# Optimization experiments

Hardware: AMD Instinct MI355X
Metric: run time of the kernel (lower is better)

## Reference

```python
import jax, jax.numpy as jnp
import numpy as np

E = 512      # embed_dim
H = 8        # num_heads
D = E // H   # head_dim = 64
R = 32       # rot_dims (partial rotary)
THETA = 10000.0


def _rope(x):
    # x: [B, H, S, D]; rotate first R dims (interleaved pairs, lucidrains-style)
    S = x.shape[-2]
    inv_freq = THETA ** (-jnp.arange(0, R, 2, dtype=jnp.float32) / R)  # [R/2]
    ang = jnp.arange(S, dtype=jnp.float32)[:, None] * inv_freq          # [S, R/2]
    c, s = jnp.cos(ang), jnp.sin(ang)
    xr, xp = x[..., :R], x[..., R:]
    x1, x2 = xr[..., 0::2], xr[..., 1::2]
    rot = jnp.stack([x1 * c - x2 * s, x1 * s + x2 * c], axis=-1).reshape(xr.shape)
    return jnp.concatenate([rot, xp], axis=-1)


def setup_inputs() -> dict:
    key = jax.random.key(0)
    k1, k2, k3, k4 = jax.random.split(key, 4)
    B, S = 4, 2048
    x = jax.random.normal(k1, (B, S, E), dtype=jnp.float32)
    input_mask = jax.random.randint(k2, (B, S), 0, 2).astype(bool)
    W_in = jax.random.normal(k3, (3 * E, E), dtype=jnp.float32) / np.sqrt(E).astype(np.float32)
    W_out = jax.random.normal(k4, (E, E), dtype=jnp.float32) / np.sqrt(E).astype(np.float32)
    return {"x": x, "input_mask": input_mask, "W_in": W_in, "W_out": W_out}


def reference(x, input_mask, W_in, W_out):
    B, S, _ = x.shape
    # fused QKV projection (Linear, no bias): x @ W_in.T -> [B,S,3E]
    qkv = (x @ W_in.T).reshape(B, S, 3, H, D).transpose(2, 0, 3, 1, 4)  # [3,B,H,S,D]
    q, k, v = qkv[0], qkv[1], qkv[2]
    q = _rope(q)
    k = _rope(k)
    # mask: causal AND (both tokens valid OR diagonal)
    causal = jnp.tril(jnp.ones((S, S), dtype=bool))
    inv = ~input_mask                                  # [B,S]
    cross = inv[:, None, :] | inv[:, :, None]          # [B,S,S]
    square = (~cross) | jnp.eye(S, dtype=bool)         # diagonal forced True
    full = causal[None, :, :] & square                 # [B,S,S]
    scores = jnp.einsum('bhsd,bhtd->bhst', q, k) / np.float32(np.sqrt(D))
    scores = jnp.where(full[:, None, :, :], scores, -jnp.inf)
    probs = jax.nn.softmax(scores, axis=-1)
    attn = jnp.einsum('bhst,bhtd->bhsd', probs, v)
    attn = attn.transpose(0, 2, 1, 3).reshape(B, S, E)
    return attn @ W_out.T
```

## Files before the change

kernel.cpp:

```cpp
#include <hip/hip_runtime.h>
#include <math.h>

#define B_ 4
#define S_ 2048
#define E_ 512
#define H_ 8
#define D_ 64

typedef short bf16x8 __attribute__((ext_vector_type(8)));
typedef float f32x4 __attribute__((ext_vector_type(4)));

__device__ inline short f2bf(float f) {
  union { float f; unsigned u; } v; v.f = f;
  unsigned r = v.u + 0x7FFF + ((v.u >> 16) & 1);
  return (short)(r >> 16);
}
__device__ inline short f2bf_fast(float f) {
  union { float f; unsigned u; } v; v.f = f;
  return (short)((v.u + 0x8000u) >> 16);
}
__device__ inline float bf2f(short s) {
  union { unsigned u; float f; } v; v.u = ((unsigned)(unsigned short)s) << 16;
  return v.f;
}

__global__ __launch_bounds__(256) void cvt_bf16(const float* __restrict__ src,
                                                short* __restrict__ dst, int n4) {
  int i = blockIdx.x * 256 + threadIdx.x;
  if (i < n4) {
    float4 f = ((const float4*)src)[i];
    short4 o;
    o.x = f2bf(f.x); o.y = f2bf(f.y); o.z = f2bf(f.z); o.w = f2bf(f.w);
    ((short4*)dst)[i] = o;
  }
}

__global__ __launch_bounds__(256) void gemm_qkv_mfma(
    const short* __restrict__ Xb,
    const short* __restrict__ Wb,
    short* __restrict__ qb, short* __restrict__ kb, short* __restrict__ vbT) {
  __shared__ __align__(16) short As[128][40];
  __shared__ __align__(16) short Bs[128][40];
  const int tid = threadIdx.x;
  const int w = tid >> 6, lane = tid & 63;
  const int l15 = lane & 15, quad = lane >> 4;
  const int wm = w & 1, wn = w >> 1;
  const int m0 = blockIdx.x * 128;
  const int n0 = blockIdx.y * 128;
  f32x4 acc[4][4];
  for (int mt = 0; mt < 4; ++mt)
    for (int nt = 0; nt < 4; ++nt) acc[mt][nt] = (f32x4){0.f, 0.f, 0.f, 0.f};

  for (int k0 = 0; k0 < E_; k0 += 32) {
    __syncthreads();
    for (int l = 0; l < 2; ++l) {
      int c = tid + 256 * l;
      int row = c >> 2, k8 = (c & 3) * 8;
      *(bf16x8*)&As[row][k8] = *(const bf16x8*)&Xb[(size_t)(m0 + row) * E_ + k0 + k8];
      *(bf16x8*)&Bs[row][k8] = *(const bf16x8*)&Wb[(size_t)(n0 + row) * E_ + k0 + k8];
    }
    __syncthreads();
    bf16x8 a[4], bfr[4];
    for (int mt = 0; mt < 4; ++mt)
      a[mt] = *(const bf16x8*)&As[wm * 64 + mt * 16 + l15][quad * 8];
    for (int nt = 0; nt < 4; ++nt)
      bfr[nt] = *(const bf16x8*)&Bs[wn * 64 + nt * 16 + l15][quad * 8];
    for (int mt = 0; mt < 4; ++mt)
      for (int nt = 0; nt < 4; ++nt)
        acc[mt][nt] = __builtin_amdgcn_mfma_f32_16x16x32_bf16(a[mt], bfr[nt], acc[mt][nt], 0, 0, 0);
  }
  const int t3 = n0 >> 9;
  for (int nt = 0; nt < 4; ++nt) {
    const int n = n0 + wn * 64 + nt * 16 + l15;
    const int h = (n >> 6) & 7;
    const int d = n & 63;
    const bool dorope = (t3 < 2) && (d < 32);
    const float sgn = (d & 1) ? 1.f : -1.f;
    const float fr = dorope ? powf(10000.f, -(float)(2 * (d >> 1)) * (1.f / 32.f)) : 0.f;
    for (int mt = 0; mt < 4; ++mt) {
      for (int i = 0; i < 4; ++i) {
        const int m = m0 + wm * 64 + mt * 16 + quad * 4 + i;
        const int b = m >> 11, s = m & (S_ - 1);
        float val = acc[mt][nt][i];
        float pv = __shfl_xor(val, 1, 64);
        float outv = val;
        if (dorope) {
          float ang = (float)s * fr;
          float sn, cs;
          sincosf(ang, &sn, &cs);
          outv = val * cs + pv * sgn * sn;
        }
        if (t3 == 2)
          vbT[((size_t)(b * 8 + h) * D_ + d) * S_ + s] = f2bf(outv);
        else {
          short* dst = (t3 == 0) ? qb : kb;
          dst[(((size_t)(b * 8 + h)) * S_ + s) * D_ + d] = f2bf(outv);
        }
      }
    }
  }
}

__global__ __launch_bounds__(256) void gemm_out_mfma(
    const short* __restrict__ Ab, const short* __restrict__ Wb,
    float* __restrict__ out) {
  __shared__ __align__(16) short As[128][40];
  __shared__ __align__(16) short Bs[128][40];
  const int tid = threadIdx.x;
  const int w = tid >> 6, lane = tid & 63;
  const int l15 = lane & 15, quad = lane >> 4;
  const int wm = w & 1, wn = w >> 1;
  const int m0 = blockIdx.x * 128;
  const int n0 = blockIdx.y * 128;
  f32x4 acc[4][4];
  for (int mt = 0; mt < 4; ++mt)
    for (int nt = 0; nt < 4; ++nt) acc[mt][nt] = (f32x4){0.f, 0.f, 0.f, 0.f};

  for (int k0 = 0; k0 < E_; k0 += 32) {
    __syncthreads();
    for (int l = 0; l < 2; ++l) {
      int c = tid + 256 * l;
      int row = c >> 2, k8 = (c & 3) * 8;
      *(bf16x8*)&As[row][k8] = *(const bf16x8*)&Ab[(size_t)(m0 + row) * E_ + k0 + k8];
      *(bf16x8*)&Bs[row][k8] = *(const bf16x8*)&Wb[(size_t)(n0 + row) * E_ + k0 + k8];
    }
    __syncthreads();
    bf16x8 a[4], bfr[4];
    for (int mt = 0; mt < 4; ++mt)
      a[mt] = *(const bf16x8*)&As[wm * 64 + mt * 16 + l15][quad * 8];
    for (int nt = 0; nt < 4; ++nt)
      bfr[nt] = *(const bf16x8*)&Bs[wn * 64 + nt * 16 + l15][quad * 8];
    for (int mt = 0; mt < 4; ++mt)
      for (int nt = 0; nt < 4; ++nt)
        acc[mt][nt] = __builtin_amdgcn_mfma_f32_16x16x32_bf16(a[mt], bfr[nt], acc[mt][nt], 0, 0, 0);
  }
  for (int mt = 0; mt < 4; ++mt)
    for (int nt = 0; nt < 4; ++nt) {
      const int n = n0 + wn * 64 + nt * 16 + l15;
      for (int i = 0; i < 4; ++i) {
        const int m = m0 + wm * 64 + mt * 16 + quad * 4 + i;
        out[(size_t)m * E_ + n] = acc[mt][nt][i];
      }
    }
}

__global__ __launch_bounds__(256) void flash_mfma(
    const short* __restrict__ qb, const short* __restrict__ kb,
    const short* __restrict__ vbT, const int* __restrict__ maskp,
    short* __restrict__ pb0, short* __restrict__ pb1,
    float* __restrict__ lb0, float* __restrict__ lb1,
    short* __restrict__ ob) {
  __shared__ __align__(16) short Ks[64][72];
  __shared__ __align__(16) short VT[64][72];
  __shared__ __align__(16) short Pl[4][16][72];
  __shared__ float kbias[64];
  const int tid = threadIdx.x;
  const int w = tid >> 6, lane = tid & 63;
  const int l15 = lane & 15, quad = lane >> 4;
  const int bid = blockIdx.x;
  const int u = bid & 7, v = bid >> 3;
  const int bh = (u << 2) | (v & 3);
  const int w2 = v >> 2;
  const int pair = w2 & 15;
  const int kh = w2 >> 4;
  const int b = bh >> 3, hd = bh & 7;
  const short* qbase = qb + (size_t)bh * S_ * D_;
  const short* kbase = kb + (size_t)bh * S_ * D_;
  const short* vtb   = vbT + (size_t)bh * D_ * S_;
  short* PB = kh ? pb1 : pb0;
  float* LB = kh ? lb1 : lb0;
  const float c2 = 0.1803368801f;
  bf16x8 ones;
  for (int j = 0; j < 8; ++j) ones[j] = (short)0x3F80;

  for (int seg = 0; seg < 2; ++seg) {
    const int qt = (seg == 0) ? pair : 31 - pair;
    const int r0 = qt * 64;
    const int mid = (qt + 2) >> 1;
    const int lo = kh ? mid : 0;
    const int hi = kh ? (qt + 1) : mid;
    bf16x8 aq[2];
    {
      const short* qrow = qbase + (size_t)(r0 + 16 * w + l15) * D_;
      aq[0] = *(const bf16x8*)&qrow[quad * 8];
      aq[1] = *(const bf16x8*)&qrow[32 + quad * 8];
    }
    f32x4 o[4], lsum;
    for (int no = 0; no < 4; ++no) o[no] = (f32x4){0.f, 0.f, 0.f, 0.f};
    lsum = (f32x4){0.f, 0.f, 0.f, 0.f};

    for (int kt = lo; kt < hi; ++kt) {
      const int t0 = kt * 64;
      __syncthreads();
      for (int l = 0; l < 2; ++l) {
        int idx = tid + 256 * l;
        int row = idx >> 3, ch = (idx & 7) * 8;
        *(bf16x8*)&Ks[row][ch] = *(const bf16x8*)(kbase + (size_t)(t0 + row) * D_ + ch);
        *(bf16x8*)&VT[row][ch] = *(const bf16x8*)(vtb + (size_t)row * S_ + t0 + ch);
      }
      if (tid < 64)
        kbias[tid] = maskp[b * S_ + t0 + tid] ? -23.08312f : -1.0e38f;
      __syncthreads();
      f32x4 sfr[4];
      for (int nb = 0; nb < 4; ++nb) sfr[nb] = (f32x4){0.f, 0.f, 0.f, 0.f};
      for (int nb = 0; nb < 4; ++nb)
        for (int ks = 0; ks < 2; ++ks) {
          bf16x8 bk = *(const bf16x8*)&Ks[l15 + 16 * nb][32 * ks + quad * 8];
          sfr[nb] = __builtin_amdgcn_mfma_f32_16x16x32_bf16(aq[ks], bk, sfr[nb], 0, 0, 0);
        }
      if (kt < qt) {
        for (int nb = 0; nb < 4; ++nb) {
          const float bb = kbias[l15 + 16 * nb];
          for (int i = 0; i < 4; ++i)
            Pl[w][quad * 4 + i][l15 + 16 * nb] = f2bf_fast(exp2f(sfr[nb][i] * c2 + bb));
        }
      } else {
        for (int nb = 0; nb < 4; ++nb) {
          const int tg = l15 + 16 * nb;
          const float bb = kbias[l15 + 16 * nb];
          for (int i = 0; i < 4; ++i) {
            const float bbi = (tg > 16 * w + quad * 4 + i) ? -1.0e38f : bb;
            Pl[w][quad * 4 + i][l15 + 16 * nb] = f2bf_fast(exp2f(sfr[nb][i] * c2 + bbi));
          }
        }
      }
      asm volatile("s_waitcnt lgkmcnt(0)" ::: "memory");
      bf16x8 ap0 = *(const bf16x8*)&Pl[w][l15][quad * 8];
      bf16x8 ap1 = *(const bf16x8*)&Pl[w][l15][32 + quad * 8];
      for (int no = 0; no < 4; ++no) {
        bf16x8 bv0 = *(const bf16x8*)&VT[16 * no + l15][quad * 8];
        bf16x8 bv1 = *(const bf16x8*)&VT[16 * no + l15][32 + quad * 8];
        o[no] = __builtin_amdgcn_mfma_f32_16x16x32_bf16(ap0, bv0, o[no], 0, 0, 0);
        o[no] = __builtin_amdgcn_mfma_f32_16x16x32_bf16(ap1, bv1, o[no], 0, 0, 0);
      }
      lsum = __builtin_amdgcn_mfma_f32_16x16x32_bf16(ap0, ones, lsum, 0, 0, 0);
      lsum = __builtin_amdgcn_mfma_f32_16x16x32_bf16(ap1, ones, lsum, 0, 0, 0);
    }
    for (int i = 0; i < 4; ++i) {
      const int s = r0 + 16 * w + quad * 4 + i;
      const int qm = maskp[b * S_ + s];
      const size_t row = (size_t)(b * S_ + s) * E_ + hd * D_;
      if (kh == 0 && !qm) {
        for (int no = 0; no < 4; ++no) {
          const int d = l15 + 16 * no;
          ob[row + d] = vtb[(size_t)d * S_ + s];
        }
      }
      for (int no = 0; no < 4; ++no)
        PB[row + l15 + 16 * no] = f2bf(o[no][i]);
      if (l15 == 0)
        LB[bh * S_ + s] = lsum[i];
    }
  }
}

__global__ __launch_bounds__(256) void merge_kernel(
    const short* __restrict__ pb0, const short* __restrict__ pb1,
    const float* __restrict__ lb0, const float* __restrict__ lb1,
    const int* __restrict__ maskp, short* __restrict__ ob) {
  int idx = blockIdx.x * 256 + threadIdx.x;
  int m = idx >> 6, e = (idx & 63) * 8;
  if (!maskp[m]) return;
  int b = m >> 11, s = m & (S_ - 1);
  int bh = b * 8 + (e >> 6);
  float l = lb0[bh * S_ + s] + lb1[bh * S_ + s];
  float inv = 1.f / l;
  bf16x8 p0 = *(const bf16x8*)&pb0[(size_t)m * E_ + e];
  bf16x8 p1 = *(const bf16x8*)&pb1[(size_t)m * E_ + e];
  bf16x8 r;
  for (int j = 0; j < 8; ++j)
    r[j] = f2bf((bf2f(p0[j]) + bf2f(p1[j])) * inv);
  *(bf16x8*)&ob[(size_t)m * E_ + e] = r;
}

extern "C" void kernel_launch(void* const* d_in, const int* in_sizes, int n_in,
                              void* d_out, int out_size, void* d_ws, size_t ws_size,
                              hipStream_t stream) {
  const float* x    = (const float*)d_in[0];
  const int*   mask = (const int*)d_in[1];
  const float* Win  = (const float*)d_in[2];
  const float* Wout = (const float*)d_in[3];
  float* out = (float*)d_out;

  short* Xb    = (short*)d_ws;
  short* Winb  = Xb + 8192 * 512;
  short* Woutb = Winb + 1536 * 512;
  short* qb    = Woutb + 512 * 512;
  short* kb    = qb + 32 * 2048 * 64;
  short* vbT   = kb + 32 * 2048 * 64;
  short* ob    = vbT + 32 * 2048 * 64;
  short* pb0   = ob + 8192 * 512;
  short* pb1   = pb0 + 8192 * 512;
  float* lb0   = (float*)(pb1 + 8192 * 512);
  float* lb1   = lb0 + 32 * 2048;

  cvt_bf16<<<4096, 256, 0, stream>>>(x, Xb, 8192 * 512 / 4);
  cvt_bf16<<<768, 256, 0, stream>>>(Win, Winb, 1536 * 512 / 4);
  cvt_bf16<<<256, 256, 0, stream>>>(Wout, Woutb, 512 * 512 / 4);
  gemm_qkv_mfma<<<dim3(64, 12), 256, 0, stream>>>(Xb, Winb, qb, kb, vbT);
  flash_mfma<<<1024, 256, 0, stream>>>(qb, kb, vbT, mask, pb0, pb1, lb0, lb1, ob);
  merge_kernel<<<2048, 256, 0, stream>>>(pb0, pb1, lb0, lb1, mask, ob);
  gemm_out_mfma<<<dim3(64, 4), 256, 0, stream>>>(ob, Woutb, out);
}
```

Before: 178.3 us.

## Use direct-to-LDS async loads in GEMMs and merge bf16 conversion launches

Both projection GEMMs now stage A/B tiles with global_load_lds (16-byte direct-to-LDS loads) instead of register round-trips, dropping the LDS row padding to fit the contiguous layout. The three fp32-to-bf16 conversion launches are merged into one kernel, and the RoPE epilogue uses the fast __sincosf intrinsic. Removing the padding may add LDS bank conflicts on the fragment reads, and __sincosf loses accuracy for large angles (positions up to 2047). Waiting on the async loads relies on __syncthreads inserting the right vmcnt waits.

```diff
diff --git a/kernel.cpp b/kernel.cpp
--- a/kernel.cpp
+++ b/kernel.cpp
@@ -10,6 +10,13 @@
 typedef short bf16x8 __attribute__((ext_vector_type(8)));
 typedef float f32x4 __attribute__((ext_vector_type(4)));
 
+typedef __attribute__((address_space(3))) void lds_void;
+typedef const __attribute__((address_space(1))) void gbl_void;
+
+__device__ inline void async16(short* lds_base, const short* gsrc) {
+  __builtin_amdgcn_global_load_lds((gbl_void*)gsrc, (lds_void*)lds_base, 16, 0, 0);
+}
+
 __device__ inline short f2bf(float f) {
   union { float f; unsigned u; } v; v.f = f;
   unsigned r = v.u + 0x7FFF + ((v.u >> 16) & 1);
@@ -24,41 +31,53 @@
   return v.f;
 }
 
-__global__ __launch_bounds__(256) void cvt_bf16(const float* __restrict__ src,
-                                                short* __restrict__ dst, int n4) {
-  int i = blockIdx.x * 256 + threadIdx.x;
-  if (i < n4) {
-    float4 f = ((const float4*)src)[i];
-    short4 o;
-    o.x = f2bf(f.x); o.y = f2bf(f.y); o.z = f2bf(f.z); o.w = f2bf(f.w);
-    ((short4*)dst)[i] = o;
-  }
+__global__ __launch_bounds__(256) void cvt_all(
+    const float* __restrict__ x, const float* __restrict__ win,
+    const float* __restrict__ wout, short* __restrict__ xb,
+    short* __restrict__ winb, short* __restrict__ woutb) {
+  int bid = blockIdx.x;
+  const float* src; short* dst; int i;
+  if (bid < 4096)      { src = x;    dst = xb;    i = bid * 256 + threadIdx.x; }
+  else if (bid < 4864) { src = win;  dst = winb;  i = (bid - 4096) * 256 + threadIdx.x; }
+  else                 { src = wout; dst = woutb; i = (bid - 4864) * 256 + threadIdx.x; }
+  float4 f = ((const float4*)src)[i];
+  short4 o;
+  o.x = f2bf(f.x); o.y = f2bf(f.y); o.z = f2bf(f.z); o.w = f2bf(f.w);
+  ((short4*)dst)[i] = o;
 }
 
 __global__ __launch_bounds__(256) void gemm_qkv_mfma(
     const short* __restrict__ Xb,
     const short* __restrict__ Wb,
     short* __restrict__ qb, short* __restrict__ kb, short* __restrict__ vbT) {
-  __shared__ __align__(16) short As[128][40];
-  __shared__ __align__(16) short Bs[128][40];
+  __shared__ __align__(16) short As[128][32];
+  __shared__ __align__(16) short Bs[128][32];
   const int tid = threadIdx.x;
   const int w = tid >> 6, lane = tid & 63;
   const int l15 = lane & 15, quad = lane >> 4;
   const int wm = w & 1, wn = w >> 1;
   const int m0 = blockIdx.x * 128;
   const int n0 = blockIdx.y * 128;
+  const int srow = w * 32 + (lane >> 2);
+  const int scol = (lane & 3) * 8;
+  const short* gA0 = &Xb[(size_t)(m0 + srow) * E_ + scol];
+  const short* gA1 = &Xb[(size_t)(m0 + srow + 16) * E_ + scol];
+  const short* gB0 = &Wb[(size_t)(n0 + srow) * E_ + scol];
+  const short* gB1 = &Wb[(size_t)(n0 + srow + 16) * E_ + scol];
+  short* lA0 = &As[w * 32][0];
+  short* lA1 = &As[w * 32 + 16][0];
+  short* lB0 = &Bs[w * 32][0];
+  short* lB1 = &Bs[w * 32 + 16][0];
   f32x4 acc[4][4];
   for (int mt = 0; mt < 4; ++mt)
     for (int nt = 0; nt < 4; ++nt) acc[mt][nt] = (f32x4){0.f, 0.f, 0.f, 0.f};
 
   for (int k0 = 0; k0 < E_; k0 += 32) {
     __syncthreads();
-    for (int l = 0; l < 2; ++l) {
-      int c = tid + 256 * l;
-      int row = c >> 2, k8 = (c & 3) * 8;
-      *(bf16x8*)&As[row][k8] = *(const bf16x8*)&Xb[(size_t)(m0 + row) * E_ + k0 + k8];
-      *(bf16x8*)&Bs[row][k8] = *(const bf16x8*)&Wb[(size_t)(n0 + row) * E_ + k0 + k8];
-    }
+    async16(lA0, gA0 + k0);
+    async16(lA1, gA1 + k0);
+    async16(lB0, gB0 + k0);
+    async16(lB1, gB1 + k0);
     __syncthreads();
     bf16x8 a[4], bfr[4];
     for (int mt = 0; mt < 4; ++mt)
@@ -85,9 +104,8 @@
         float pv = __shfl_xor(val, 1, 64);
         float outv = val;
         if (dorope) {
-          float ang = (float)s * fr;
           float sn, cs;
-          sincosf(ang, &sn, &cs);
+          __sincosf((float)s * fr, &sn, &cs);
           outv = val * cs + pv * sgn * sn;
         }
         if (t3 == 2)
@@ -104,26 +122,34 @@
 __global__ __launch_bounds__(256) void gemm_out_mfma(
     const short* __restrict__ Ab, const short* __restrict__ Wb,
     float* __restrict__ out) {
-  __shared__ __align__(16) short As[128][40];
-  __shared__ __align__(16) short Bs[128][40];
+  __shared__ __align__(16) short As[128][32];
+  __shared__ __align__(16) short Bs[128][32];
   const int tid = threadIdx.x;
   const int w = tid >> 6, lane = tid & 63;
   const int l15 = lane & 15, quad = lane >> 4;
   const int wm = w & 1, wn = w >> 1;
   const int m0 = blockIdx.x * 128;
   const int n0 = blockIdx.y * 128;
+  const int srow = w * 32 + (lane >> 2);
+  const int scol = (lane & 3) * 8;
+  const short* gA0 = &Ab[(size_t)(m0 + srow) * E_ + scol];
+  const short* gA1 = &Ab[(size_t)(m0 + srow + 16) * E_ + scol];
+  const short* gB0 = &Wb[(size_t)(n0 + srow) * E_ + scol];
+  const short* gB1 = &Wb[(size_t)(n0 + srow + 16) * E_ + scol];
+  short* lA0 = &As[w * 32][0];
+  short* lA1 = &As[w * 32 + 16][0];
+  short* lB0 = &Bs[w * 32][0];
+  short* lB1 = &Bs[w * 32 + 16][0];
   f32x4 acc[4][4];
   for (int mt = 0; mt < 4; ++mt)
     for (int nt = 0; nt < 4; ++nt) acc[mt][nt] = (f32x4){0.f, 0.f, 0.f, 0.f};
 
   for (int k0 = 0; k0 < E_; k0 += 32) {
     __syncthreads();
-    for (int l = 0; l < 2; ++l) {
-      int c = tid + 256 * l;
-      int row = c >> 2, k8 = (c & 3) * 8;
-      *(bf16x8*)&As[row][k8] = *(const bf16x8*)&Ab[(size_t)(m0 + row) * E_ + k0 + k8];
-      *(bf16x8*)&Bs[row][k8] = *(const bf16x8*)&Wb[(size_t)(n0 + row) * E_ + k0 + k8];
-    }
+    async16(lA0, gA0 + k0);
+    async16(lA1, gA1 + k0);
+    async16(lB0, gB0 + k0);
+    async16(lB1, gB1 + k0);
     __syncthreads();
     bf16x8 a[4], bfr[4];
     for (int mt = 0; mt < 4; ++mt)
@@ -294,9 +320,7 @@
   float* lb0   = (float*)(pb1 + 8192 * 512);
   float* lb1   = lb0 + 32 * 2048;
 
-  cvt_bf16<<<4096, 256, 0, stream>>>(x, Xb, 8192 * 512 / 4);
-  cvt_bf16<<<768, 256, 0, stream>>>(Win, Winb, 1536 * 512 / 4);
-  cvt_bf16<<<256, 256, 0, stream>>>(Wout, Woutb, 512 * 512 / 4);
+  cvt_all<<<5120, 256, 0, stream>>>(x, Win, Wout, Xb, Winb, Woutb);
   gemm_qkv_mfma<<<dim3(64, 12), 256, 0, stream>>>(Xb, Winb, qb, kb, vbT);
   flash_mfma<<<1024, 256, 0, stream>>>(qb, kb, vbT, mask, pb0, pb1, lb0, lb1, ob);
   merge_kernel<<<2048, 256, 0, stream>>>(pb0, pb1, lb0, lb1, mask, ob);
```

Result: slower. 270.7 us (+51.8%).
